# Kernel tuning notes

Measured on AMD Instinct MI355X. Metric: run time of the kernel, lower is better.

The kernel has to match this reference:

```python
import jax, jax.numpy as jnp
import numpy as np

NUM_INPUTS, NUM_HIDDEN, NUM_OUTPUTS = 512, 1024, 35
T, B = 100, 512
N_HID_LAYERS = 4  # number of hidden Leaky layers (num_layers)
SLOPE = 25.0      # snntorch surrogate.fast_sigmoid default slope
BETA, THR = 0.95, 1.0


@jax.custom_vjp
def spike(x):
    # Heaviside forward, fast-sigmoid surrogate backward
    return (x > 0).astype(x.dtype)

def _spike_fwd(x):
    return (x > 0).astype(x.dtype), x

def _spike_bwd(x, g):
    return (g / (SLOPE * jnp.abs(x) + 1.0) ** 2,)

spike.defvjp(_spike_fwd, _spike_bwd)


def leaky(x, mem, beta, thr):
    # snntorch Leaky, reset_mechanism='subtract':
    # reset computed from PREVIOUS mem (detached), then decay+input, then fire
    reset = jax.lax.stop_gradient((mem - thr > 0).astype(x.dtype))
    mem = jnp.clip(beta, 0.0, 1.0) * mem + x - reset * thr
    spk = spike(mem - thr)
    return spk, mem


def setup_inputs() -> dict:
    key = jax.random.key(0)
    ks = jax.random.split(key, 8)
    data = jax.random.normal(ks[0], (T, B, NUM_INPUTS), dtype=jnp.float32)
    s_in = 1.0 / np.sqrt(NUM_INPUTS)
    s_h = 1.0 / np.sqrt(NUM_HIDDEN)
    W_in = jax.random.uniform(ks[1], (NUM_HIDDEN, NUM_INPUTS), minval=-s_in, maxval=s_in, dtype=jnp.float32)
    b_in = jax.random.uniform(ks[2], (NUM_HIDDEN,), minval=-s_in, maxval=s_in, dtype=jnp.float32)
    W_h = jax.random.uniform(ks[3], (N_HID_LAYERS - 1, NUM_HIDDEN, NUM_HIDDEN), minval=-s_h, maxval=s_h, dtype=jnp.float32)
    b_h = jax.random.uniform(ks[4], (N_HID_LAYERS - 1, NUM_HIDDEN), minval=-s_h, maxval=s_h, dtype=jnp.float32)
    W_out = jax.random.uniform(ks[5], (NUM_OUTPUTS, NUM_HIDDEN), minval=-s_h, maxval=s_h, dtype=jnp.float32)
    b_out = jax.random.uniform(ks[6], (NUM_OUTPUTS,), minval=-s_h, maxval=s_h, dtype=jnp.float32)
    # learn_beta/learn_threshold: each Leaky holds its own (identically initialized) params
    beta_h = jnp.full((N_HID_LAYERS, NUM_HIDDEN), BETA, dtype=jnp.float32)
    thr_h = jnp.full((N_HID_LAYERS, NUM_HIDDEN), THR, dtype=jnp.float32)
    beta_o = jnp.full((NUM_OUTPUTS,), BETA, dtype=jnp.float32)
    thr_o = jnp.full((NUM_OUTPUTS,), THR, dtype=jnp.float32)
    return {"data": data, "W_in": W_in, "b_in": b_in, "W_h": W_h, "b_h": b_h,
            "W_out": W_out, "b_out": b_out, "beta_h": beta_h, "thr_h": thr_h,
            "beta_o": beta_o, "thr_o": thr_o, "timestep": 100}


def reference(data, W_in, b_in, W_h, b_h, W_out, b_out, beta_h, thr_h, beta_o, thr_o, timestep):
    n_hid = beta_h.shape[0]
    Bsz = data.shape[1]

    def step(mems, x_t):
        new_mems = []
        x = x_t @ W_in.T + b_in
        x, m = leaky(x, mems[0], beta_h[0], thr_h[0])
        new_mems.append(m)
        for i in range(n_hid - 1):
            z = x @ W_h[i].T + b_h[i]
            x, m = leaky(z, mems[i + 1], beta_h[i + 1], thr_h[i + 1])
            new_mems.append(m)
        z = x @ W_out.T + b_out
        spk, m = leaky(z, mems[n_hid], beta_o, thr_o)
        new_mems.append(m)
        return tuple(new_mems), spk

    mems0 = tuple([jnp.zeros((Bsz, NUM_HIDDEN), dtype=data.dtype) for _ in range(n_hid)]
                  + [jnp.zeros((Bsz, NUM_OUTPUTS), dtype=data.dtype)])
    _, spk_rec = jax.lax.scan(step, mems0, data[:timestep])
    return spk_rec  # [T, B, num_outputs]
```

## Files before the change

### kernel.cpp

```cpp
#include <hip/hip_runtime.h>
#include <hip/hip_bf16.h>


#define NB 512
#define NH 1024
#define NI 512
#define NO 35
#define TT 100
#define NT 8
#define BITFRAME 16384

typedef __bf16 bf16x8 __attribute__((ext_vector_type(8)));
typedef float f32x4 __attribute__((ext_vector_type(4)));
typedef int   i32x4 __attribute__((ext_vector_type(4)));

__device__ __forceinline__ size_t tiled_off(int row, int k, int KT) {
    return ((size_t)((row >> 4) * KT + (k >> 5)) * 64
            + (row & 15) + (((k >> 3) & 3) << 4)) * 8 + (k & 7);
}

__device__ __forceinline__ void leaky_upd(float zin, float mprev, float be, float th,
                                          float& mnew, float& spk) {
    float rs = (mprev - th > 0.0f) ? th : 0.0f;
    float bc = fminf(fmaxf(be, 0.0f), 1.0f);
    mnew = bc * mprev + zin - rs;
    spk  = (mnew - th > 0.0f) ? 1.0f : 0.0f;
}

#define WS_MEM123   0u
#define WS_MEM0     6291456u
#define WS_MEMO     8388608u
#define WS_FLAGS    8486912u
#define WS_GEN      8487936u
#define WS_RING0    8488192u
#define WS_RING1    9536768u
#define WS_RING2    10585344u
#define WS_RING3    11633920u
#define WS_W8       12682496u
#define WS_WIT      25265408u
#define WS_WOT      28411136u
#define WS_Z0       28706048u
#define STEP_BYTES  2097152u

__global__ __launch_bounds__(256)
void split_weights_i8(const float* __restrict__ W_h, signed char* __restrict__ W8) {
    const int id = blockIdx.x * 256 + threadIdx.x;
    const int layer = id >> 16;
    const int rem = id & 65535;
    const int n = rem >> 6;
    const int k0 = (rem & 63) << 4;
    const float* src = W_h + ((size_t)layer * NH + n) * NH + k0;
    const int kq = k0 >> 4;
    const int ck = kq >> 2;
    const int lane = (n & 15) | ((kq & 3) << 4);
    signed char* dstL = W8 + (size_t)layer * 4 * NH * NH;
    const size_t gb = ((size_t)(n >> 4) * 16 + ck) * 1024 + lane * 16;

    signed char q1[16], q2[16], q3[16], q4[16];
    #pragma unroll
    for (int j = 0; j < 16; ++j) {
        float w = src[j];
        float f1 = rintf(w * 0x1p11f);   float r1 = w  - f1 * 0x1p-11f;
        float f2 = rintf(r1 * 0x1p18f);  float r2 = r1 - f2 * 0x1p-18f;
        float f3 = rintf(r2 * 0x1p25f);  float r3 = r2 - f3 * 0x1p-25f;
        float f4 = rintf(r3 * 0x1p32f);
        q1[j] = (signed char)(int)f1; q2[j] = (signed char)(int)f2;
        q3[j] = (signed char)(int)f3; q4[j] = (signed char)(int)f4;
    }
    #pragma unroll
    for (int j = 0; j < 16; ++j) {
        dstL[(size_t)0 * 64 * 16384 + gb + j] = q1[j];
        dstL[(size_t)1 * 64 * 16384 + gb + j] = q2[j];
        dstL[(size_t)2 * 64 * 16384 + gb + j] = q3[j];
        dstL[(size_t)3 * 64 * 16384 + gb + j] = q4[j];
    }
}

__global__ __launch_bounds__(256)
void split_win(const float* __restrict__ W_in, __bf16* __restrict__ Wi_t) {
    const int id = blockIdx.x * 256 + threadIdx.x;
    const int n = id >> 6;
    const int k0 = (id & 63) << 3;
    const float* src = W_in + (size_t)n * NI + k0;
    const size_t PS = (size_t)NH * NI;
    const size_t off = tiled_off(n, k0, 16);
    bf16x8 p1, p2, p3;
    #pragma unroll
    for (int j = 0; j < 8; ++j) {
        float w = src[j];
        __bf16 a = (__bf16)w;  float r1 = w - (float)a;
        __bf16 b = (__bf16)r1; float r2 = r1 - (float)b;
        __bf16 c = (__bf16)r2;
        p1[j] = a; p2[j] = b; p3[j] = c;
    }
    *reinterpret_cast<bf16x8*>(Wi_t + 0 * PS + off) = p1;
    *reinterpret_cast<bf16x8*>(Wi_t + 1 * PS + off) = p2;
    *reinterpret_cast<bf16x8*>(Wi_t + 2 * PS + off) = p3;
}

__global__ __launch_bounds__(256)
void split_wout(const float* __restrict__ W_out, __bf16* __restrict__ Wo_t) {
    const int id = blockIdx.x * 256 + threadIdx.x;
    if (id >= 48 * 128) return;
    const int o = id >> 7;
    const int k0 = (id & 127) << 3;
    const size_t PS = (size_t)48 * NH;
    const size_t off = tiled_off(o, k0, 32);
    bf16x8 p1 = {}, p2 = {}, p3 = {};
    if (o < NO) {
        const float* src = W_out + (size_t)o * NH + k0;
        #pragma unroll
        for (int j = 0; j < 8; ++j) {
            float w = src[j];
            __bf16 a = (__bf16)w;  float r1 = w - (float)a;
            __bf16 b = (__bf16)r1; float r2 = r1 - (float)b;
            __bf16 c = (__bf16)r2;
            p1[j] = a; p2[j] = b; p3[j] = c;
        }
    }
    *reinterpret_cast<bf16x8*>(Wo_t + 0 * PS + off) = p1;
    *reinterpret_cast<bf16x8*>(Wo_t + 1 * PS + off) = p2;
    *reinterpret_cast<bf16x8*>(Wo_t + 2 * PS + off) = p3;
}

__global__ __launch_bounds__(256)
void z0_gemm(const float* __restrict__ X,
             const __bf16* __restrict__ Wi_t,
             const float* __restrict__ bias,
             float* __restrict__ Z0)
{
    const int tid = threadIdx.x;
    const int lane = tid & 63;
    const int w = tid >> 6;
    const int wm = w >> 1, wn = w & 1;
    const int m_base = blockIdx.y * 64 + wm * 32;
    const int n_base = blockIdx.x * 64 + wn * 32;
    const size_t PS = (size_t)NH * NI;

    f32x4 acc[2][2] = {};
    const float* asrc[2];
    #pragma unroll
    for (int mt = 0; mt < 2; ++mt)
        asrc[mt] = X + (size_t)(m_base + mt * 16 + (lane & 15)) * NI + ((lane >> 4) << 3);

    float4 c0[2], c1[2];
    #pragma unroll
    for (int mt = 0; mt < 2; ++mt) {
        c0[mt] = *reinterpret_cast<const float4*>(asrc[mt]);
        c1[mt] = *reinterpret_cast<const float4*>(asrc[mt] + 4);
    }

    for (int kt = 0; kt < 16; ++kt) {
        float4 n0[2], n1[2];
        if (kt < 15) {
            #pragma unroll
            for (int mt = 0; mt < 2; ++mt) {
                n0[mt] = *reinterpret_cast<const float4*>(asrc[mt] + (kt + 1) * 32);
                n1[mt] = *reinterpret_cast<const float4*>(asrc[mt] + (kt + 1) * 32 + 4);
            }
        }
        bf16x8 a1[2], a2[2], a3[2];
        #pragma unroll
        for (int mt = 0; mt < 2; ++mt) {
            float xv[8] = {c0[mt].x, c0[mt].y, c0[mt].z, c0[mt].w,
                           c1[mt].x, c1[mt].y, c1[mt].z, c1[mt].w};
            #pragma unroll
            for (int j = 0; j < 8; ++j) {
                float x = xv[j];
                __bf16 h1 = (__bf16)x;  float r1 = x - (float)h1;
                __bf16 h2 = (__bf16)r1; float r2 = r1 - (float)h2;
                __bf16 h3 = (__bf16)r2;
                a1[mt][j] = h1; a2[mt][j] = h2; a3[mt][j] = h3;
            }
        }
        #pragma unroll
        for (int nt = 0; nt < 2; ++nt) {
            const size_t bo = ((size_t)(((n_base >> 4) + nt) * 16 + kt) * 64 + lane) * 8;
            bf16x8 b1 = *reinterpret_cast<const bf16x8*>(Wi_t + bo);
            bf16x8 b2 = *reinterpret_cast<const bf16x8*>(Wi_t + PS + bo);
            bf16x8 b3 = *reinterpret_cast<const bf16x8*>(Wi_t + 2 * PS + bo);
            #pragma unroll
            for (int mt = 0; mt < 2; ++mt) {
                f32x4 A = acc[mt][nt];
                A = __builtin_amdgcn_mfma_f32_16x16x32_bf16(a1[mt], b1, A, 0, 0, 0);
                A = __builtin_amdgcn_mfma_f32_16x16x32_bf16(a1[mt], b2, A, 0, 0, 0);
                A = __builtin_amdgcn_mfma_f32_16x16x32_bf16(a2[mt], b1, A, 0, 0, 0);
                A = __builtin_amdgcn_mfma_f32_16x16x32_bf16(a2[mt], b2, A, 0, 0, 0);
                A = __builtin_amdgcn_mfma_f32_16x16x32_bf16(a1[mt], b3, A, 0, 0, 0);
                A = __builtin_amdgcn_mfma_f32_16x16x32_bf16(a3[mt], b1, A, 0, 0, 0);
                acc[mt][nt] = A;
            }
        }
        if (kt < 15) {
            #pragma unroll
            for (int mt = 0; mt < 2; ++mt) { c0[mt] = n0[mt]; c1[mt] = n1[mt]; }
        }
    }

    const int c = lane & 15;
    const int r0 = (lane >> 4) * 4;
    #pragma unroll
    for (int nt = 0; nt < 2; ++nt) {
        const int n = n_base + nt * 16 + c;
        const float bi = bias[n];
        #pragma unroll
        for (int mt = 0; mt < 2; ++mt) {
            #pragma unroll
            for (int r = 0; r < 4; ++r) {
                const int m = m_base + mt * 16 + r0 + r;
                const int tl = m >> 9, b = m & 511;
                Z0[(size_t)tl * (NB * NH) + tiled_off(b, n, 32)] = acc[mt][nt][r] + bi;
            }
        }
    }
}

__device__ __forceinline__ void gridbar(int* flags, int* gen, int target) {
    __syncthreads();
    if (threadIdx.x == 0) {
        __builtin_amdgcn_fence(__ATOMIC_RELEASE, "agent");
        __hip_atomic_store(&flags[blockIdx.x], target, __ATOMIC_RELAXED, __HIP_MEMORY_SCOPE_AGENT);
    }
    if (blockIdx.x == 0) {
        if (threadIdx.x < 64) {
            const int l = threadIdx.x;
            for (;;) {
                int v0 = __hip_atomic_load(&flags[l],       __ATOMIC_RELAXED, __HIP_MEMORY_SCOPE_AGENT);
                int v1 = __hip_atomic_load(&flags[l + 64],  __ATOMIC_RELAXED, __HIP_MEMORY_SCOPE_AGENT);
                int v2 = __hip_atomic_load(&flags[l + 128], __ATOMIC_RELAXED, __HIP_MEMORY_SCOPE_AGENT);
                int v3 = __hip_atomic_load(&flags[l + 192], __ATOMIC_RELAXED, __HIP_MEMORY_SCOPE_AGENT);
                int mn = min(min(v0, v1), min(v2, v3));
                if (__all(mn >= target)) break;
                __builtin_amdgcn_s_sleep(1);
            }
        }
        __syncthreads();
        if (threadIdx.x == 0) {
            __builtin_amdgcn_fence(__ATOMIC_ACQ_REL, "agent");
            __hip_atomic_store(gen, target, __ATOMIC_RELAXED, __HIP_MEMORY_SCOPE_AGENT);
        }
    } else if (threadIdx.x == 0) {
        while (__hip_atomic_load(gen, __ATOMIC_RELAXED, __HIP_MEMORY_SCOPE_AGENT) < target)
            __builtin_amdgcn_s_sleep(2);
    }
    __syncthreads();
    __builtin_amdgcn_fence(__ATOMIC_ACQUIRE, "agent");
}

template<int NS>
__device__ __forceinline__ void hidden_run_i8(
    const unsigned int* const* Xp, unsigned short* const* Yp,
    const signed char* Wl, int cs, int rh, int w, int lane,
    float (&memr)[2][2][4], const float (&bi)[2], const float (&be)[2],
    const float (&th)[2])
{
    const int row  = lane & 15;
    const int lg   = lane >> 4;
    const int wsel = lg >> 1;
    const int hsel = (lg & 1) * 16;

    i32x4 acc[NS][2][2][4] = {};

    unsigned int bw[NS][2];
    #pragma unroll
    for (int q = 0; q < NS; ++q)
        #pragma unroll
        for (int i = 0; i < 2; ++i)
            bw[q][i] = Xp[q][((rh * 16 + w * 2 + i) * 32 + wsel) * 16 + row];

    i32x4 bf[8];
    #pragma unroll
    for (int pn = 0; pn < 8; ++pn)
        bf[pn] = *reinterpret_cast<const i32x4*>(Wl + pn * 16384 + lane * 16);

    for (int ck = 0; ck < 16; ++ck) {
        unsigned int nb[NS][2];
        i32x4 nf[8];
        if (ck < 15) {
            #pragma unroll
            for (int pn = 0; pn < 8; ++pn)
                nf[pn] = *reinterpret_cast<const i32x4*>(
                    Wl + pn * 16384 + (ck + 1) * 1024 + lane * 16);
            #pragma unroll
            for (int q = 0; q < NS; ++q)
                #pragma unroll
                for (int i = 0; i < 2; ++i)
                    nb[q][i] = Xp[q][((rh * 16 + w * 2 + i) * 32 + (ck + 1) * 2 + wsel) * 16 + row];
        }

        #pragma unroll
        for (int q = 0; q < NS; ++q) {
            #pragma unroll
            for (int i = 0; i < 2; ++i) {
                unsigned int half = (bw[q][i] >> hsel) & 0xFFFFu;
                union { unsigned int u[4]; i32x4 v; } a;
                a.u[0] = (((half      ) & 0xFu) * 0x204081u) & 0x01010101u;
                a.u[1] = (((half >>  4) & 0xFu) * 0x204081u) & 0x01010101u;
                a.u[2] = (((half >>  8) & 0xFu) * 0x204081u) & 0x01010101u;
                a.u[3] = (((half >> 12) & 0xFu) * 0x204081u) & 0x01010101u;
                #pragma unroll
                for (int nt = 0; nt < 2; ++nt)
                    #pragma unroll
                    for (int p = 0; p < 4; ++p)
                        acc[q][i][nt][p] = __builtin_amdgcn_mfma_i32_16x16x64_i8(
                            a.v, bf[p * 2 + nt], acc[q][i][nt][p], 0, 0, 0);
            }
        }
        if (ck < 15) {
            #pragma unroll
            for (int q = 0; q < NS; ++q) { bw[q][0] = nb[q][0]; bw[q][1] = nb[q][1]; }
            #pragma unroll
            for (int pn = 0; pn < 8; ++pn) bf[pn] = nf[pn];
        }
    }

    #pragma unroll
    for (int q = 0; q < NS; ++q) {
        #pragma unroll
        for (int i = 0; i < 2; ++i) {
            #pragma unroll
            for (int nt = 0; nt < 2; ++nt) {
                #pragma unroll
                for (int r = 0; r < 4; ++r) {
                    float z = (float)acc[q][i][nt][3][r] * 0x1p-32f
                            + (float)acc[q][i][nt][2][r] * 0x1p-25f;
                    z += (float)acc[q][i][nt][1][r] * 0x1p-18f;
                    z += (float)acc[q][i][nt][0][r] * 0x1p-11f;
                    float mn, sp;
                    leaky_upd(z + bi[nt], memr[i][nt][r], be[nt], th[nt], mn, sp);
                    memr[i][nt][r] = mn;
                    unsigned long long bal = __ballot(sp != 0.0f);
                    if ((lane & 15) == 0) {
                        const int rr = (lane >> 4) * 4 + r;
                        Yp[q][(((rh * 16 + w * 2 + i) * 32 + cs) * 16 + rr) * 2 + nt] =
                            (unsigned short)((bal >> ((lane >> 4) * 16)) & 0xFFFFu);
                    }
                }
            }
        }
    }
}

__global__ __launch_bounds__(512, 1)
void snn_pipe(const float* __restrict__ Z0,
              const signed char* __restrict__ W8,
              const __bf16* __restrict__ Wo_t,
              const float* __restrict__ b_h,
              const float* __restrict__ b_out,
              const float* __restrict__ beta_h,
              const float* __restrict__ thr_h,
              const float* __restrict__ beta_o,
              const float* __restrict__ thr_o,
              float* __restrict__ mem123,
              float* __restrict__ mem0_g,
              float* __restrict__ memo_g,
              unsigned int* __restrict__ ring0, unsigned int* __restrict__ ring1,
              unsigned int* __restrict__ ring2, unsigned int* __restrict__ ring3,
              float* __restrict__ out,
              int* __restrict__ flags, int* __restrict__ gen,
              int t0, int tc)
{
    __shared__ signed char Wl[8 * 16 * 1024];
    __shared__ unsigned long long lut[16];

    const int blk  = blockIdx.x;
    const int tid  = threadIdx.x;
    const int lane = tid & 63;
    const int w    = tid >> 6;

    if (tid < 16) {
        unsigned int lo = ((tid & 1) ? 0x3F80u : 0u) | ((tid & 2) ? 0x3F800000u : 0u);
        unsigned int hi = ((tid & 4) ? 0x3F80u : 0u) | ((tid & 8) ? 0x3F800000u : 0u);
        lut[tid] = ((unsigned long long)hi << 32) | lo;
    }

    const int G = (tc + NT - 1) / NT;

    if (blk < 192) {
        const int ell = blk >> 6;
        const int cs  = (blk & 63) >> 1;
        const int rh  = blk & 1;
        {
            const signed char* Wsrc = W8 + (size_t)ell * 4 * NH * NH;
            for (int idx = tid; idx < 8 * 1024; idx += 512) {
                const int pn = idx >> 10, off = idx & 1023;
                const int p = pn >> 1, nt = pn & 1;
                *reinterpret_cast<int4*>(Wl + pn * 16384 + off * 16) =
                    *reinterpret_cast<const int4*>(
                        Wsrc + (size_t)(p * 64 + cs * 2 + nt) * 16384 + off * 16);
            }
        }

        const int c = lane & 15;
        const int r0v = (lane >> 4) * 4;
        float* memg = mem123 + (size_t)ell * (NB * NH);
        float bi[2], be[2], th[2];
        #pragma unroll
        for (int nt = 0; nt < 2; ++nt) {
            const int n = cs * 32 + nt * 16 + c;
            bi[nt] = b_h[ell * NH + n];
            be[nt] = beta_h[(ell + 1) * NH + n];
            th[nt] = thr_h[(ell + 1) * NH + n];
        }
        float memr[2][2][4];
        #pragma unroll
        for (int i = 0; i < 2; ++i)
            #pragma unroll
            for (int nt = 0; nt < 2; ++nt)
                #pragma unroll
                for (int r = 0; r < 4; ++r)
                    memr[i][nt][r] = memg[(size_t)(rh * 256 + (w * 2 + i) * 16 + r0v + r) * NH
                                          + cs * 32 + nt * 16 + c];

        const unsigned int* rin = (ell == 0) ? ring0 : (ell == 1) ? ring1 : ring2;
        unsigned int* rout      = (ell == 0) ? ring1 : (ell == 1) ? ring2 : ring3;

        __syncthreads();

        for (int p = 0; p < G + 4; ++p) {
            const int g = p - 1 - ell;
            if (g >= 0 && g < G) {
                const int sbase = g * NT;
                const int send  = (sbase + NT < tc) ? sbase + NT : tc;
                const int slot0 = (g & 1) * NT;
                int s = sbase;
                while (s < send) {
                    const int base = slot0 + (s - sbase);
                    const unsigned int* Xp[2];
                    unsigned short* Yp[2];
                    if (send - s >= 2) {
                        #pragma unroll
                        for (int q = 0; q < 2; ++q) {
                            Xp[q] = rin + (size_t)(base + q) * BITFRAME;
                            Yp[q] = (unsigned short*)(rout + (size_t)(base + q) * BITFRAME);
                        }
                        hidden_run_i8<2>(Xp, Yp, Wl, cs, rh, w, lane, memr, bi, be, th);
                        s += 2;
                    } else {
                        Xp[0] = rin + (size_t)base * BITFRAME;
                        Yp[0] = (unsigned short*)(rout + (size_t)base * BITFRAME);
                        hidden_run_i8<1>(Xp, Yp, Wl, cs, rh, w, lane, memr, bi, be, th);
                        s += 1;
                    }
                }
            }
            gridbar(flags, gen, p + 1);
        }

        #pragma unroll
        for (int i = 0; i < 2; ++i)
            #pragma unroll
            for (int nt = 0; nt < 2; ++nt)
                #pragma unroll
                for (int r = 0; r < 4; ++r)
                    memg[(size_t)(rh * 256 + (w * 2 + i) * 16 + r0v + r) * NH
                         + cs * 32 + nt * 16 + c] = memr[i][nt][r];
    } else if (blk < 224) {
        const bool outw = (w < 3);
        const int omt = blk - 192;
        const int ont = w;
        const int c = lane & 15, r0v = (lane >> 4) * 4;
        const int row = lane & 15, sh2 = (lane >> 4) * 8;
        const int oo = ont * 16 + c;
        const size_t OPS = (size_t)48 * NH;
        float mo[4] = {0.f, 0.f, 0.f, 0.f};
        float obi = 0.f, obe = 0.f, oth = 1.f;
        if (outw && oo < NO) {
            obi = b_out[oo]; obe = beta_o[oo]; oth = thr_o[oo];
            #pragma unroll
            for (int r = 0; r < 4; ++r) mo[r] = memo_g[(omt * 16 + r0v + r) * NO + oo];
        }
        __syncthreads();

        for (int p = 0; p < G + 4; ++p) {
            if (outw) {
                const int go = p - 4;
                if (go >= 0 && go < G) {
                    const int sbase = go * NT;
                    const int send  = (sbase + NT < tc) ? sbase + NT : tc;
                    const int slot0 = (go & 1) * NT;
                    for (int s = sbase; s < send; ++s) {
                        const unsigned int* Xw =
                            ring3 + (size_t)(slot0 + s - sbase) * BITFRAME;
                        f32x4 acc = {};
                        for (int kt = 0; kt < 32; ++kt) {
                            unsigned int by = (Xw[(omt * 32 + kt) * 16 + row] >> sh2) & 0xffu;
                            union { unsigned long long u[2]; bf16x8 v; } a;
                            a.u[0] = lut[by & 15u];
                            a.u[1] = lut[by >> 4];
                            const size_t bo = ((size_t)(ont * 32 + kt) * 64 + lane) * 8;
                            bf16x8 q1 = *reinterpret_cast<const bf16x8*>(Wo_t + bo);
                            bf16x8 q2 = *reinterpret_cast<const bf16x8*>(Wo_t + OPS + bo);
                            bf16x8 q3 = *reinterpret_cast<const bf16x8*>(Wo_t + 2 * OPS + bo);
                            acc = __builtin_amdgcn_mfma_f32_16x16x32_bf16(a.v, q1, acc, 0, 0, 0);
                            acc = __builtin_amdgcn_mfma_f32_16x16x32_bf16(a.v, q2, acc, 0, 0, 0);
                            acc = __builtin_amdgcn_mfma_f32_16x16x32_bf16(a.v, q3, acc, 0, 0, 0);
                        }
                        if (oo < NO) {
                            #pragma unroll
                            for (int r = 0; r < 4; ++r) {
                                float mn, sp;
                                leaky_upd(acc[r] + obi, mo[r], obe, oth, mn, sp);
                                mo[r] = mn;
                                out[((size_t)(t0 + s) * NB + omt * 16 + r0v + r) * NO + oo] = sp;
                            }
                        }
                    }
                }
            }
            gridbar(flags, gen, p + 1);
        }

        if (outw && oo < NO) {
            #pragma unroll
            for (int r = 0; r < 4; ++r) memo_g[(omt * 16 + r0v + r) * NO + oo] = mo[r];
        }
    } else {
        const int wi   = (blk - 224) * 512 + tid;
        const int mtb  = wi >> 9;
        const int ktb  = (wi >> 4) & 31;
        const int i0   = (mtb * 32 + ktb) * 512 + (wi & 15) * 8;

        float m0[32], be0[32], th0[32];
        #pragma unroll
        for (int byt = 0; byt < 4; ++byt)
            #pragma unroll
            for (int j = 0; j < 8; ++j) {
                m0[byt * 8 + j]  = mem0_g[i0 + byt * 128 + j];
                be0[byt * 8 + j] = beta_h[ktb * 32 + byt * 8 + j];
                th0[byt * 8 + j] = thr_h[ktb * 32 + byt * 8 + j];
            }
        __syncthreads();

        for (int p = 0; p < G + 4; ++p) {
            if (p < G) {
                const int sbase = p * NT;
                const int send  = (sbase + NT < tc) ? sbase + NT : tc;
                const int slot0 = (p & 1) * NT;
                for (int s = sbase; s < send; ++s) {
                    const float* zs = Z0 + (size_t)s * (NB * NH) + i0;
                    float4 zv[8];
                    #pragma unroll
                    for (int byt = 0; byt < 4; ++byt) {
                        zv[byt * 2]     = *reinterpret_cast<const float4*>(zs + byt * 128);
                        zv[byt * 2 + 1] = *reinterpret_cast<const float4*>(zs + byt * 128 + 4);
                    }
                    unsigned int bits = 0;
                    #pragma unroll
                    for (int e = 0; e < 32; ++e) {
                        float z = reinterpret_cast<const float*>(zv)[e];
                        float mn, sp;
                        leaky_upd(z, m0[e], be0[e], th0[e], mn, sp);
                        m0[e] = mn;
                        bits |= (sp != 0.0f ? 1u : 0u) << e;
                    }
                    ring0[(size_t)(slot0 + s - sbase) * BITFRAME + wi] = bits;
                }
            }
            gridbar(flags, gen, p + 1);
        }

        #pragma unroll
        for (int byt = 0; byt < 4; ++byt)
            #pragma unroll
            for (int j = 0; j < 8; ++j)
                mem0_g[i0 + byt * 128 + j] = m0[byt * 8 + j];
    }
}

extern "C" void kernel_launch(void* const* d_in, const int* in_sizes, int n_in,
                              void* d_out, int out_size, void* d_ws, size_t ws_size,
                              hipStream_t stream) {
    const float* data   = (const float*)d_in[0];
    const float* W_in   = (const float*)d_in[1];
    const float* b_in   = (const float*)d_in[2];
    const float* W_h    = (const float*)d_in[3];
    const float* b_h    = (const float*)d_in[4];
    const float* W_out  = (const float*)d_in[5];
    const float* b_out  = (const float*)d_in[6];
    const float* beta_h = (const float*)d_in[7];
    const float* thr_h  = (const float*)d_in[8];
    const float* beta_o = (const float*)d_in[9];
    const float* thr_o  = (const float*)d_in[10];
    float* out = (float*)d_out;

    char* ws = (char*)d_ws;
    float*        mem123 = (float*)(ws + WS_MEM123);
    float*        mem0_g = (float*)(ws + WS_MEM0);
    float*        memo_g = (float*)(ws + WS_MEMO);
    int*          flags  = (int*)(ws + WS_FLAGS);
    int*          gen    = (int*)(ws + WS_GEN);
    unsigned int* ring0  = (unsigned int*)(ws + WS_RING0);
    unsigned int* ring1  = (unsigned int*)(ws + WS_RING1);
    unsigned int* ring2  = (unsigned int*)(ws + WS_RING2);
    unsigned int* ring3  = (unsigned int*)(ws + WS_RING3);
    signed char*  W8     = (signed char*)(ws + WS_W8);
    __bf16*       Wi_t   = (__bf16*)(ws + WS_WIT);
    __bf16*       Wo_t   = (__bf16*)(ws + WS_WOT);
    float*        Z0     = (float*)(ws + WS_Z0);

    size_t avail = (ws_size > WS_Z0) ? (ws_size - WS_Z0) / STEP_BYTES : 1;
    int Tc = (int)(avail < 1 ? 1 : (avail > TT ? TT : avail));

    hipMemsetAsync(ws, 0, WS_FLAGS, stream);
    split_weights_i8<<<dim3(768), dim3(256), 0, stream>>>(W_h, W8);
    split_win<<<dim3(256), dim3(256), 0, stream>>>(W_in, Wi_t);
    split_wout<<<dim3(24), dim3(256), 0, stream>>>(W_out, Wo_t);

    for (int t0c = 0; t0c < TT; t0c += Tc) {
        const int tcc = (TT - t0c < Tc) ? (TT - t0c) : Tc;
        z0_gemm<<<dim3(NH / 64, tcc * (NB / 64)), dim3(256), 0, stream>>>(
            data + (size_t)t0c * NB * NI, Wi_t, b_in, Z0);
        hipMemsetAsync(ws + WS_FLAGS, 0, 1280, stream);
        snn_pipe<<<dim3(256), dim3(512), 0, stream>>>(
            Z0, W8, Wo_t, b_h, b_out, beta_h, thr_h, beta_o, thr_o,
            mem123, mem0_g, memo_g, ring0, ring1, ring2, ring3, out,
            flags, gen, t0c, tcc);
    }
}
```

Measured before the change: 1.657 ms.

## Fuse input-layer GEMM into persistent pipeline kernel via double-buffered Z0 ring

New measurement: 5.249 ms. 3.17x slower.

```diff
diff --git a/kernel.cpp b/kernel.cpp
--- a/kernel.cpp
+++ b/kernel.cpp
@@ -9,6 +9,7 @@
 #define TT 100
 #define NT 8
 #define BITFRAME 16384
+#define FRAME_F  (NB * NH)
 
 typedef __bf16 bf16x8 __attribute__((ext_vector_type(8)));
 typedef float f32x4 __attribute__((ext_vector_type(4)));
@@ -39,8 +40,7 @@
 #define WS_W8       12682496u
 #define WS_WIT      25265408u
 #define WS_WOT      28411136u
-#define WS_Z0       28706048u
-#define STEP_BYTES  2097152u
+#define WS_Z0R      28706048u
 
 __global__ __launch_bounds__(256)
 void split_weights_i8(const float* __restrict__ W_h, signed char* __restrict__ W8) {
@@ -123,20 +123,13 @@
     *reinterpret_cast<bf16x8*>(Wo_t + 2 * PS + off) = p3;
 }
 
-__global__ __launch_bounds__(256)
-void z0_gemm(const float* __restrict__ X,
-             const __bf16* __restrict__ Wi_t,
-             const float* __restrict__ bias,
-             float* __restrict__ Z0)
+__device__ __forceinline__ void z0_tile(const float* __restrict__ X,
+                                        const __bf16* __restrict__ Wi_t,
+                                        const float* __restrict__ bias,
+                                        float* __restrict__ dst,
+                                        int m_base, int n_base, int lane)
 {
-    const int tid = threadIdx.x;
-    const int lane = tid & 63;
-    const int w = tid >> 6;
-    const int wm = w >> 1, wn = w & 1;
-    const int m_base = blockIdx.y * 64 + wm * 32;
-    const int n_base = blockIdx.x * 64 + wn * 32;
     const size_t PS = (size_t)NH * NI;
-
     f32x4 acc[2][2] = {};
     const float* asrc[2];
     #pragma unroll
@@ -208,8 +201,7 @@
             #pragma unroll
             for (int r = 0; r < 4; ++r) {
                 const int m = m_base + mt * 16 + r0 + r;
-                const int tl = m >> 9, b = m & 511;
-                Z0[(size_t)tl * (NB * NH) + tiled_off(b, n, 32)] = acc[mt][nt][r] + bi;
+                dst[tiled_off(m, n, 32)] = acc[mt][nt][r] + bi;
             }
         }
     }
@@ -342,7 +334,9 @@
 }
 
 __global__ __launch_bounds__(512, 1)
-void snn_pipe(const float* __restrict__ Z0,
+void snn_pipe(const float* __restrict__ data,
+              const __bf16* __restrict__ Wi_t,
+              const float* __restrict__ b_in,
               const signed char* __restrict__ W8,
               const __bf16* __restrict__ Wo_t,
               const float* __restrict__ b_h,
@@ -354,11 +348,12 @@
               float* __restrict__ mem123,
               float* __restrict__ mem0_g,
               float* __restrict__ memo_g,
+              float* __restrict__ Z0ring,
               unsigned int* __restrict__ ring0, unsigned int* __restrict__ ring1,
               unsigned int* __restrict__ ring2, unsigned int* __restrict__ ring3,
               float* __restrict__ out,
               int* __restrict__ flags, int* __restrict__ gen,
-              int t0, int tc)
+              int tc)
 {
     __shared__ signed char Wl[8 * 16 * 1024];
     __shared__ unsigned long long lut[16];
@@ -417,8 +412,8 @@
 
         __syncthreads();
 
-        for (int p = 0; p < G + 4; ++p) {
-            const int g = p - 1 - ell;
+        for (int p = 0; p < G + 5; ++p) {
+            const int g = p - 2 - ell;
             if (g >= 0 && g < G) {
                 const int sbase = g * NT;
                 const int send  = (sbase + NT < tc) ? sbase + NT : tc;
@@ -472,9 +467,9 @@
         }
         __syncthreads();
 
-        for (int p = 0; p < G + 4; ++p) {
+        for (int p = 0; p < G + 5; ++p) {
             if (outw) {
-                const int go = p - 4;
+                const int go = p - 5;
                 if (go >= 0 && go < G) {
                     const int sbase = go * NT;
                     const int send  = (sbase + NT < tc) ? sbase + NT : tc;
@@ -502,7 +497,7 @@
                                 float mn, sp;
                                 leaky_upd(acc[r] + obi, mo[r], obe, oth, mn, sp);
                                 mo[r] = mn;
-                                out[((size_t)(t0 + s) * NB + omt * 16 + r0v + r) * NO + oo] = sp;
+                                out[((size_t)s * NB + omt * 16 + r0v + r) * NO + oo] = sp;
                             }
                         }
                     }
@@ -520,6 +515,7 @@
         const int mtb  = wi >> 9;
         const int ktb  = (wi >> 4) & 31;
         const int i0   = (mtb * 32 + ktb) * 512 + (wi & 15) * 8;
+        const int gw   = (blk - 224) * 8 + w;
 
         float m0[32], be0[32], th0[32];
         #pragma unroll
@@ -532,13 +528,27 @@
             }
         __syncthreads();
 
-        for (int p = 0; p < G + 4; ++p) {
+        for (int p = 0; p < G + 5; ++p) {
             if (p < G) {
                 const int sbase = p * NT;
+                const int nst = ((sbase + NT < tc) ? NT : tc - sbase);
+                float* slot = Z0ring + (size_t)(p & 1) * NT * FRAME_F;
+                for (int idx = gw; idx < nst * 512; idx += 256) {
+                    const int sl = idx >> 9;
+                    const int rem = idx & 511;
+                    z0_tile(data + (size_t)(sbase + sl) * NB * NI, Wi_t, b_in,
+                            slot + (size_t)sl * FRAME_F,
+                            (rem >> 5) * 32, (rem & 31) * 32, lane);
+                }
+            }
+            const int gl = p - 1;
+            if (gl >= 0 && gl < G) {
+                const int sbase = gl * NT;
                 const int send  = (sbase + NT < tc) ? sbase + NT : tc;
-                const int slot0 = (p & 1) * NT;
+                const int slot0 = (gl & 1) * NT;
+                const float* slotZ = Z0ring + (size_t)(gl & 1) * NT * FRAME_F;
                 for (int s = sbase; s < send; ++s) {
-                    const float* zs = Z0 + (size_t)s * (NB * NH) + i0;
+                    const float* zs = slotZ + (size_t)(s - sbase) * FRAME_F + i0;
                     float4 zv[8];
                     #pragma unroll
                     for (int byt = 0; byt < 4; ++byt) {
@@ -597,24 +607,18 @@
     signed char*  W8     = (signed char*)(ws + WS_W8);
     __bf16*       Wi_t   = (__bf16*)(ws + WS_WIT);
     __bf16*       Wo_t   = (__bf16*)(ws + WS_WOT);
-    float*        Z0     = (float*)(ws + WS_Z0);
-
-    size_t avail = (ws_size > WS_Z0) ? (ws_size - WS_Z0) / STEP_BYTES : 1;
-    int Tc = (int)(avail < 1 ? 1 : (avail > TT ? TT : avail));
+    float*        Z0ring = (float*)(ws + WS_Z0R);
 
     hipMemsetAsync(ws, 0, WS_FLAGS, stream);
+    hipMemsetAsync(ws + WS_FLAGS, 0, 1280, stream);
     split_weights_i8<<<dim3(768), dim3(256), 0, stream>>>(W_h, W8);
     split_win<<<dim3(256), dim3(256), 0, stream>>>(W_in, Wi_t);
     split_wout<<<dim3(24), dim3(256), 0, stream>>>(W_out, Wo_t);
 
-    for (int t0c = 0; t0c < TT; t0c += Tc) {
-        const int tcc = (TT - t0c < Tc) ? (TT - t0c) : Tc;
-        z0_gemm<<<dim3(NH / 64, tcc * (NB / 64)), dim3(256), 0, stream>>>(
-            data + (size_t)t0c * NB * NI, Wi_t, b_in, Z0);
-        hipMemsetAsync(ws + WS_FLAGS, 0, 1280, stream);
-        snn_pipe<<<dim3(256), dim3(512), 0, stream>>>(
-            Z0, W8, Wo_t, b_h, b_out, beta_h, thr_h, beta_o, thr_o,
-            mem123, mem0_g, memo_g, ring0, ring1, ring2, ring3, out,
-            flags, gen, t0c, tcc);
-    }
-}
+    snn_pipe<<<dim3(256), dim3(512), 0, stream>>>(
+        data, Wi_t, b_in, W8, Wo_t, b_h, b_out,
+        beta_h, thr_h, beta_o, thr_o,
+        mem123, mem0_g, memo_g, Z0ring,
+        ring0, ring1, ring2, ring3, out,
+        flags, gen, TT);
+}
```
